# Optimization experiments

Measured on AMD Instinct MI355X. Metric: run time of the kernel, lower is better.

## Reference

```python
import jax, jax.numpy as jnp
import numpy as np

INF = 1e38  # matches torch source constant


def setup_inputs() -> dict:
    key = jax.random.key(0)
    k1, k2, k3 = jax.random.split(key, 3)
    B, N, D = 16, 2048, 512
    query = jax.random.normal(k1, (B, N, D), dtype=jnp.float32)
    # nn.Linear(dims, dims, bias=False): weight [out, in] = [D, D]
    W_in = jax.random.normal(k2, (D, D), dtype=jnp.float32) * (1.0 / np.sqrt(D))
    # nn.Linear(2*dims, dims, bias=False): weight [D, 2D]
    W_out = jax.random.normal(k3, (D, 2 * D), dtype=jnp.float32) * (1.0 / np.sqrt(2 * D))
    return {"query": query, "W_in": W_in, "W_out": W_out}


def reference(query, W_in, W_out):
    B, N, D = query.shape
    # linear_in: y = x @ W^T
    q = jnp.einsum("bnd,ed->bne", query, W_in)  # [B, N, D]
    # full QK^T scores
    scores = jnp.einsum("bnd,bmd->bnm", q, q)  # [B, N, N]
    # torch: scores[:, triu_mask] = -INF  -> mask upper triangle INCLUDING diagonal
    mask = jnp.triu(jnp.ones((N, N), dtype=bool))
    scores = jnp.where(mask, -INF, scores)
    weights = jax.nn.softmax(scores, axis=-1)
    # row 0 is all -INF -> softmax gives uniform; torch zeroes it explicitly
    weights = weights.at[:, 0, :].set(0.0)
    mix = jnp.einsum("bnm,bmd->bnd", weights, q)  # [B, N, D]
    combined = jnp.concatenate([mix, q], axis=-1)  # [B, N, 2D]
    # linear_out (no activation since activation=None)
    output = jnp.einsum("bnc,dc->bnd", combined, W_out)  # [B, N, D]
    return output
```

## Files before the change

kernel.cpp:

```cpp
#include <hip/hip_runtime.h>

typedef _Float16 f16;
typedef _Float16 half8 __attribute__((ext_vector_type(8)));
typedef _Float16 half4 __attribute__((ext_vector_type(4)));
typedef float floatx4 __attribute__((ext_vector_type(4)));

#define MFMA16(a, b, c) __builtin_amdgcn_mfma_f32_16x16x32_f16(a, b, c, 0, 0, 0)

#define PHASE_WAIT_4()  do { asm volatile("s_waitcnt vmcnt(4)" ::: "memory"); \
    __builtin_amdgcn_sched_barrier(0); __builtin_amdgcn_s_barrier(); } while (0)
#define PHASE_WAIT_0()  do { asm volatile("s_waitcnt vmcnt(0)" ::: "memory"); \
    __builtin_amdgcn_sched_barrier(0); __builtin_amdgcn_s_barrier(); } while (0)

__device__ __forceinline__ void gload16(const void* g, void* l) {
    __builtin_amdgcn_global_load_lds((const __attribute__((address_space(1))) void*)g,
                                     (__attribute__((address_space(3))) void*)l, 16, 0, 0);
}


__global__ __launch_bounds__(256) void k_cvt(const float* __restrict__ query,
                                             const float* __restrict__ Wi,
                                             const float* __restrict__ Wo,
                                             f16* __restrict__ q16,
                                             f16* __restrict__ W16)
{
    int i = blockIdx.x * 256 + threadIdx.x;
    const float4* src;
    f16* dst;
    if (i < 4194304) { src = (const float4*)query + i; dst = q16 + (size_t)i * 4; }
    else if (i < 4259840) { int j = i - 4194304; src = (const float4*)Wi + j; dst = W16 + (size_t)j * 4; }
    else { int j = i - 4259840; src = (const float4*)Wo + j; dst = W16 + 262144 + (size_t)j * 4; }
    float4 v = *src;
    half4 h = {(f16)v.x, (f16)v.y, (f16)v.z, (f16)v.w};
    *reinterpret_cast<half4*>(dst) = h;
}

__global__ __launch_bounds__(512, 4) void k_qin(const f16* __restrict__ q16,
                                                const f16* __restrict__ W16,
                                                f16* __restrict__ comb,
                                                f16* __restrict__ qT)
{
    __shared__ char sm[65536];
    const int tid = threadIdx.x, lane = tid & 63, w = tid >> 6;
    const int l15 = lane & 15, quad = lane >> 4;
    const int id = blockIdx.x, xcd = id & 7, u = id >> 3;
    const int mbase = (xcd * 32 + (u >> 2)) * 128;
    const int nbase = (u & 3) * 128;
    const int wm = (w & 1) * 64, wn = (w >> 1) * 32;
    const int ia = (w & 1) * 4, jb = (w >> 1) * 2;

    floatx4 acc[4][2];
#pragma unroll
    for (int i = 0; i < 4; ++i)
#pragma unroll
        for (int j = 0; j < 2; ++j) acc[i][j] = (floatx4)0.f;

    auto STAGE = [&](int k0, int bsel) {
        f16* At = (f16*)(sm + bsel * 32768);
        f16* Bt = At + 8192;
#pragma unroll
        for (int jr = 0; jr < 2; ++jr) {
            int bi = jr * 8 + w, i2 = bi >> 1, s = bi & 1;
            gload16(q16 + (size_t)(mbase + i2 * 16 + l15) * 512 + k0 + s * 32 + quad * 8, At + bi * 512);
            gload16(W16 + (size_t)(nbase + i2 * 16 + l15) * 512 + k0 + s * 32 + quad * 8, Bt + bi * 512);
        }
    };

    STAGE(0, 0);
    STAGE(64, 1);
    for (int it = 0; it < 8; ++it) {
        const int cur = it & 1;
        if (it < 7) PHASE_WAIT_4(); else PHASE_WAIT_0();
        f16* At = (f16*)(sm + cur * 32768);
        f16* Bt = At + 8192;
#pragma unroll
        for (int s = 0; s < 2; ++s) {
            half8 a[4], bf[2];
#pragma unroll
            for (int i = 0; i < 4; ++i)
                a[i] = *reinterpret_cast<half8*>(At + ((ia + i) * 2 + s) * 512 + lane * 8);
#pragma unroll
            for (int j = 0; j < 2; ++j)
                bf[j] = *reinterpret_cast<half8*>(Bt + ((jb + j) * 2 + s) * 512 + lane * 8);
#pragma unroll
            for (int i = 0; i < 4; ++i)
#pragma unroll
                for (int j = 0; j < 2; ++j)
                    acc[i][j] = MFMA16(a[i], bf[j], acc[i][j]);
        }
        __builtin_amdgcn_s_barrier();
        if (it + 2 < 8) STAGE((it + 2) * 64, cur);
    }
    const int bb = mbase >> 11, tb = mbase & 2047;
    f16* ct = (f16*)sm;
#pragma unroll
    for (int i = 0; i < 4; ++i)
#pragma unroll
        for (int j = 0; j < 2; ++j)
#pragma unroll
            for (int r = 0; r < 4; ++r)
                ct[(wm + i * 16 + quad * 4 + r) * 136 + wn + j * 16 + l15] = (f16)acc[i][j][r];
    __syncthreads();
#pragma unroll
    for (int it = 0; it < 4; ++it) {
        int c = it * 512 + tid, r = c >> 4, c8 = (c & 15) << 3;
        *reinterpret_cast<half8*>(comb + (size_t)(mbase + r) * 1024 + 512 + nbase + c8) =
            *reinterpret_cast<half8*>(ct + r * 136 + c8);
    }
    __syncthreads();
#pragma unroll
    for (int i = 0; i < 4; ++i)
#pragma unroll
        for (int j = 0; j < 2; ++j) {
            half4 h = {(f16)acc[i][j][0], (f16)acc[i][j][1], (f16)acc[i][j][2], (f16)acc[i][j][3]};
            *reinterpret_cast<half4*>(ct + (wn + j * 16 + l15) * 136 + wm + i * 16 + quad * 4) = h;
        }
    __syncthreads();
#pragma unroll
    for (int it = 0; it < 4; ++it) {
        int c = it * 512 + tid, dd = c >> 4, tc = (c & 15) << 3;
        *reinterpret_cast<half8*>(qT + ((size_t)bb * 512 + nbase + dd) * 2048 + tb + tc) =
            *reinterpret_cast<half8*>(ct + dd * 136 + tc);
    }
}

__global__ __launch_bounds__(512, 4) void k_sgemmsm(const f16* __restrict__ comb,
                                                    f16* __restrict__ Pd,
                                                    float* __restrict__ Mt,
                                                    float* __restrict__ Lt)
{
    __shared__ char sm[65536];
    const int tid = threadIdx.x, lane = tid & 63, w = tid >> 6;
    const int l15 = lane & 15, quad = lane >> 4;
    const int wm = (w & 1) * 64, wn = (w >> 1) * 32;
    const int ia = (w & 1) * 4, jb = (w >> 1) * 2;

    int bx = blockIdx.y, mt = 0;
    while ((mt + 1) * (mt + 2) / 2 <= bx) ++mt;
    const int nt = bx - mt * (mt + 1) / 2;
    const int b = blockIdx.x;
    const f16* qa = comb + ((size_t)b * 2048 + mt * 128) * 1024 + 512;
    const f16* qb = comb + ((size_t)b * 2048 + nt * 128) * 1024 + 512;

    floatx4 acc[4][2];
#pragma unroll
    for (int i = 0; i < 4; ++i)
#pragma unroll
        for (int j = 0; j < 2; ++j) acc[i][j] = (floatx4)0.f;

    auto STAGE = [&](int k0, int bsel) {
        f16* At = (f16*)(sm + bsel * 32768);
        f16* Bt = At + 8192;
#pragma unroll
        for (int jr = 0; jr < 2; ++jr) {
            int bi = jr * 8 + w, i2 = bi >> 1, s = bi & 1;
            gload16(qa + (size_t)(i2 * 16 + l15) * 1024 + k0 + s * 32 + quad * 8, At + bi * 512);
            gload16(qb + (size_t)(i2 * 16 + l15) * 1024 + k0 + s * 32 + quad * 8, Bt + bi * 512);
        }
    };

    STAGE(0, 0);
    STAGE(64, 1);
    for (int it = 0; it < 8; ++it) {
        const int cur = it & 1;
        if (it < 7) PHASE_WAIT_4(); else PHASE_WAIT_0();
        f16* At = (f16*)(sm + cur * 32768);
        f16* Bt = At + 8192;
#pragma unroll
        for (int s = 0; s < 2; ++s) {
            half8 a[4], bf[2];
#pragma unroll
            for (int i = 0; i < 4; ++i)
                a[i] = *reinterpret_cast<half8*>(At + ((ia + i) * 2 + s) * 512 + lane * 8);
#pragma unroll
            for (int j = 0; j < 2; ++j)
                bf[j] = *reinterpret_cast<half8*>(Bt + ((jb + j) * 2 + s) * 512 + lane * 8);
#pragma unroll
            for (int i = 0; i < 4; ++i)
#pragma unroll
                for (int j = 0; j < 2; ++j)
                    acc[i][j] = MFMA16(a[i], bf[j], acc[i][j]);
        }
        __builtin_amdgcn_s_barrier();
        if (it + 2 < 8) STAGE((it + 2) * 64, cur);
    }

    const bool diag = (nt == mt);
    f16* ct = (f16*)sm;
    float* redm = (float*)(sm + 34816);
    float* reds = (float*)(sm + 36864);
    const int hb = w & 1;

    float wmax[4][4];
#pragma unroll
    for (int i = 0; i < 4; ++i)
#pragma unroll
        for (int r = 0; r < 4; ++r) {
            const int rowl = wm + i * 16 + quad * 4 + r;
            float mm = -1e38f;
#pragma unroll
            for (int j = 0; j < 2; ++j) {
                float v = acc[i][j][r];
                if (diag && (wn + j * 16 + l15) >= rowl) v = -1e38f;
                mm = fmaxf(mm, v);
            }
            mm = fmaxf(mm, __shfl_xor(mm, 1));
            mm = fmaxf(mm, __shfl_xor(mm, 2));
            mm = fmaxf(mm, __shfl_xor(mm, 4));
            mm = fmaxf(mm, __shfl_xor(mm, 8));
            wmax[i][r] = mm;
        }
    if (l15 == 0)
#pragma unroll
        for (int i = 0; i < 4; ++i)
#pragma unroll
            for (int r = 0; r < 4; ++r)
                redm[w * 64 + i * 16 + quad * 4 + r] = wmax[i][r];
    __syncthreads();

#pragma unroll
    for (int i = 0; i < 4; ++i)
#pragma unroll
        for (int r = 0; r < 4; ++r) {
            const int idx = i * 16 + quad * 4 + r;
            const int rowl = wm + idx;
            const float m = fmaxf(fmaxf(redm[hb * 64 + idx], redm[(hb + 2) * 64 + idx]),
                                  fmaxf(redm[(hb + 4) * 64 + idx], redm[(hb + 6) * 64 + idx]));
            float ssum = 0.f;
#pragma unroll
            for (int j = 0; j < 2; ++j) {
                const int col = wn + j * 16 + l15;
                const bool valid = !diag || (col < rowl);
                float e = valid ? __expf(acc[i][j][r] - m) : 0.f;
                ssum += e;
                ct[rowl * 136 + col] = (f16)e;
            }
            ssum += __shfl_xor(ssum, 1);
            ssum += __shfl_xor(ssum, 2);
            ssum += __shfl_xor(ssum, 4);
            ssum += __shfl_xor(ssum, 8);
            wmax[i][r] = ssum;
        }
    if (l15 == 0)
#pragma unroll
        for (int i = 0; i < 4; ++i)
#pragma unroll
            for (int r = 0; r < 4; ++r)
                reds[w * 64 + i * 16 + quad * 4 + r] = wmax[i][r];
    __syncthreads();

    if (tid < 128) {
        const int h2 = tid >> 6, i2 = tid & 63;
        const float mm = fmaxf(fmaxf(redm[h2 * 64 + i2], redm[(h2 + 2) * 64 + i2]),
                               fmaxf(redm[(h2 + 4) * 64 + i2], redm[(h2 + 6) * 64 + i2]));
        const float ll = (reds[h2 * 64 + i2] + reds[(h2 + 2) * 64 + i2])
                       + (reds[(h2 + 4) * 64 + i2] + reds[(h2 + 6) * 64 + i2]);
        const size_t o = (((size_t)b * 16 + nt) << 11) + mt * 128 + tid;
        Mt[o] = mm;
        Lt[o] = ll;
    }
    f16* Pt = Pd + ((size_t)(b * 136 + bx) << 14);
#pragma unroll
    for (int itp = 0; itp < 4; ++itp) {
        int c = itp * 512 + tid, r_ = c >> 4, c8 = (c & 15) << 3;
        *reinterpret_cast<half8*>(Pt + r_ * 128 + c8) =
            *reinterpret_cast<half8*>(ct + r_ * 136 + c8);
    }
}

__global__ __launch_bounds__(256) void k_stats(float* Mt, const float* __restrict__ Lt)
{
    const int b = blockIdx.x, row = blockIdx.y * 256 + threadIdx.x;
    const int mtr = row >> 7;
    float mv[16], lv[16];
    for (int t = 0; t <= mtr; ++t) {
        const size_t o = (((size_t)b * 16 + t) << 11) + row;
        mv[t] = Mt[o];
        lv[t] = Lt[o];
    }
    float M = -1e38f;
    for (int t = 0; t <= mtr; ++t) M = fmaxf(M, mv[t]);
    float l = 0.f;
    for (int t = 0; t <= mtr; ++t) l += lv[t] * __expf(mv[t] - M);
    const float invl = (l > 0.f) ? 1.f / l : 0.f;
    for (int t = 0; t <= mtr; ++t)
        Mt[(((size_t)b * 16 + t) << 11) + row] = __expf(mv[t] - M) * invl;
}

__global__ __launch_bounds__(256) void k_pscale(f16* __restrict__ Pd,
                                               const float* __restrict__ Ft)
{
    int bx = blockIdx.y, mt = 0;
    while ((mt + 1) * (mt + 2) / 2 <= bx) ++mt;
    const int nt = bx - mt * (mt + 1) / 2;
    const int b = blockIdx.x;
    const int tid = threadIdx.x;
    const int row = tid >> 1, c0 = (tid & 1) * 64;
    const float Fv = Ft[(((size_t)b * 16 + nt) << 11) + mt * 128 + row];
    f16* Pt = Pd + ((size_t)(b * 136 + bx) << 14) + (size_t)row * 128 + c0;
#pragma unroll
    for (int c = 0; c < 8; ++c) {
        half8 h = *reinterpret_cast<half8*>(Pt + c * 8);
#pragma unroll
        for (int e = 0; e < 8; ++e) h[e] = (f16)((float)h[e] * Fv);
        *reinterpret_cast<half8*>(Pt + c * 8) = h;
    }
}

__global__ __launch_bounds__(512, 4) void k_pv(const f16* __restrict__ Pd,
                                               const f16* __restrict__ qT,
                                               f16* __restrict__ comb)
{
    __shared__ char sm[65536];
    const int tid = threadIdx.x, lane = tid & 63, w = tid >> 6;
    const int l15 = lane & 15, quad = lane >> 4;
    const int wm = (w & 1) * 64, wn = (w >> 1) * 32;
    const int ia = (w & 1) * 4, jb = (w >> 1) * 2;
    const int id = blockIdx.x;
    const int p = id & 7, nb = (id >> 3) & 3, b = id >> 5;
    const f16* Pdb = Pd + ((size_t)b * 136 << 14);
    const f16* qTb = qT + ((size_t)b * 512 + nb * 128) * 2048;

    for (int t = 0; t < 2; ++t) {
        const int mt = t ? (15 - p) : p;
        const int tb0 = mt * (mt + 1) / 2;
        const int kit = (mt + 1) * 2;

        floatx4 acc[4][2];
#pragma unroll
        for (int i = 0; i < 4; ++i)
#pragma unroll
            for (int j = 0; j < 2; ++j) acc[i][j] = (floatx4)0.f;

        auto STAGE = [&](int it, int bsel) {
            f16* At = (f16*)(sm + bsel * 32768);
            f16* Bt = At + 8192;
            const int k0 = it * 64;
#pragma unroll
            for (int jr = 0; jr < 2; ++jr) {
                int bi = jr * 8 + w, i2 = bi >> 1, s = bi & 1;
                gload16(Pdb + ((size_t)(tb0 + (k0 >> 7)) << 14) + (size_t)(i2 * 16 + l15) * 128
                            + (k0 & 64) + s * 32 + quad * 8,
                        At + bi * 512);
                gload16(qTb + (size_t)(i2 * 16 + l15) * 2048 + k0 + s * 32 + quad * 8, Bt + bi * 512);
            }
        };

        STAGE(0, 0);
        STAGE(1, 1);
        for (int it = 0; it < kit; ++it) {
            const int cur = it & 1;
            if (it < kit - 1) PHASE_WAIT_4(); else PHASE_WAIT_0();
            f16* At = (f16*)(sm + cur * 32768);
            f16* Bt = At + 8192;
#pragma unroll
            for (int s = 0; s < 2; ++s) {
                half8 a[4], bf[2];
#pragma unroll
                for (int i = 0; i < 4; ++i)
                    a[i] = *reinterpret_cast<half8*>(At + ((ia + i) * 2 + s) * 512 + lane * 8);
#pragma unroll
                for (int j = 0; j < 2; ++j)
                    bf[j] = *reinterpret_cast<half8*>(Bt + ((jb + j) * 2 + s) * 512 + lane * 8);
#pragma unroll
                for (int i = 0; i < 4; ++i)
#pragma unroll
                    for (int j = 0; j < 2; ++j)
                        acc[i][j] = MFMA16(a[i], bf[j], acc[i][j]);
            }
            __builtin_amdgcn_s_barrier();
            if (it + 2 < kit) STAGE(it + 2, cur);
        }

        f16* ct = (f16*)sm;
#pragma unroll
        for (int i = 0; i < 4; ++i)
#pragma unroll
            for (int j = 0; j < 2; ++j)
#pragma unroll
                for (int r = 0; r < 4; ++r)
                    ct[(wm + i * 16 + quad * 4 + r) * 136 + wn + j * 16 + l15] = (f16)acc[i][j][r];
        __syncthreads();
#pragma unroll
        for (int it = 0; it < 4; ++it) {
            int c = it * 512 + tid, r = c >> 4, c8 = (c & 15) << 3;
            *reinterpret_cast<half8*>(comb + ((size_t)b * 2048 + mt * 128 + r) * 1024 + nb * 128 + c8) =
                *reinterpret_cast<half8*>(ct + r * 136 + c8);
        }
        __syncthreads();
    }
}

__global__ __launch_bounds__(512, 4) void k_out(const f16* __restrict__ comb,
                                                const f16* __restrict__ Wo16,
                                                float* __restrict__ out)
{
    __shared__ char sm[65536];
    const int tid = threadIdx.x, lane = tid & 63, w = tid >> 6;
    const int l15 = lane & 15, quad = lane >> 4;
    const int id = blockIdx.x, xcd = id & 7, u = id >> 3;
    const int mbase = (xcd * 32 + (u >> 2)) * 128;
    const int nbase = (u & 3) * 128;
    const int wn = (w >> 1) * 32;
    const int ia = (w & 1) * 4, jb = (w >> 1) * 2;

    floatx4 acc[4][2];
#pragma unroll
    for (int i = 0; i < 4; ++i)
#pragma unroll
        for (int j = 0; j < 2; ++j) acc[i][j] = (floatx4)0.f;

    auto STAGE = [&](int k0, int bsel) {
        f16* At = (f16*)(sm + bsel * 32768);
        f16* Bt = At + 8192;
#pragma unroll
        for (int jr = 0; jr < 2; ++jr) {
            int bi = jr * 8 + w, i2 = bi >> 1, s = bi & 1;
            gload16(comb + (size_t)(mbase + i2 * 16 + l15) * 1024 + k0 + s * 32 + quad * 8,
                    At + bi * 512);
            gload16(Wo16 + (size_t)(nbase + i2 * 16 + l15) * 1024 + k0 + s * 32 + quad * 8,
                    Bt + bi * 512);
        }
    };

    STAGE(0, 0);
    STAGE(64, 1);
    for (int it = 0; it < 16; ++it) {
        const int cur = it & 1;
        if (it < 15) PHASE_WAIT_4(); else PHASE_WAIT_0();
        f16* At = (f16*)(sm + cur * 32768);
        f16* Bt = At + 8192;
#pragma unroll
        for (int s = 0; s < 2; ++s) {
            half8 a[4], bf[2];
#pragma unroll
            for (int i = 0; i < 4; ++i)
                a[i] = *reinterpret_cast<half8*>(At + ((ia + i) * 2 + s) * 512 + lane * 8);
#pragma unroll
            for (int j = 0; j < 2; ++j)
                bf[j] = *reinterpret_cast<half8*>(Bt + ((jb + j) * 2 + s) * 512 + lane * 8);
#pragma unroll
            for (int i = 0; i < 4; ++i)
#pragma unroll
                for (int j = 0; j < 2; ++j)
                    acc[i][j] = MFMA16(a[i], bf[j], acc[i][j]);
        }
        __builtin_amdgcn_s_barrier();
        if (it + 2 < 16) STAGE((it + 2) * 64, cur);
    }
    float* cf = (float*)sm;
    for (int pass = 0; pass < 2; ++pass) {
        __syncthreads();
        if ((w & 1) == pass) {
#pragma unroll
            for (int i = 0; i < 4; ++i)
#pragma unroll
                for (int j = 0; j < 2; ++j)
#pragma unroll
                    for (int r = 0; r < 4; ++r)
                        cf[(i * 16 + quad * 4 + r) * 132 + wn + j * 16 + l15] = acc[i][j][r];
        }
        __syncthreads();
#pragma unroll
        for (int it = 0; it < 4; ++it) {
            int c = it * 512 + tid, row = c >> 5, c4 = (c & 31) << 2;
            __builtin_nontemporal_store(
                *reinterpret_cast<floatx4*>(cf + row * 132 + c4),
                reinterpret_cast<floatx4*>(out + (size_t)(mbase + pass * 64 + row) * 512 + nbase + c4));
        }
    }
}

extern "C" void kernel_launch(void* const* d_in, const int* in_sizes, int n_in,
                              void* d_out, int out_size, void* d_ws, size_t ws_size,
                              hipStream_t stream)
{
    const float* query = (const float*)d_in[0];
    const float* W_in  = (const float*)d_in[1];
    const float* W_out = (const float*)d_in[2];
    float* out = (float*)d_out;

    const size_t XOFF = 102236160ull;
    f16* comb = (f16*)d_ws;
    f16* qT   = comb + (size_t)32768 * 1024;
    f16* W16  = qT + (size_t)16 * 512 * 2048;
    f16* q16  = (f16*)((char*)d_ws + XOFF);
    f16* Pd   = (f16*)((char*)d_ws + XOFF);
    float* Mt = (float*)((char*)d_ws + XOFF + 71303168ull);
    float* Lt = (float*)((char*)d_ws + XOFF + 73400320ull);

    k_cvt<<<17152, 256, 0, stream>>>(query, W_in, W_out, q16, W16);
    k_qin<<<1024, 512, 0, stream>>>(q16, W16, comb, qT);
    k_sgemmsm<<<dim3(16, 136), 512, 0, stream>>>(comb, Pd, Mt, Lt);
    k_stats<<<dim3(16, 8), 256, 0, stream>>>(Mt, Lt);
    k_pscale<<<dim3(16, 136), 256, 0, stream>>>(Pd, Mt);
    k_pv<<<512, 512, 0, stream>>>(Pd, qT, comb);
    k_out<<<1024, 512, 0, stream>>>(comb, W16 + 262144, out);
}
```

Measured before the change: 408.4 us.

## Fuse softmax row rescaling into PV GEMM and remap blocks for XCD locality

Removes the separate k_pscale pass that read and rewrote the whole P matrix. The per-tile softmax correction factors now go into LDS, and each 128-column K tile's partial accumulator is scaled and folded into a second accumulator inside k_pv. The score and PV kernels also remap block indices so each batch's blocks land on the same XCD, which should improve L2 reuse. In exchange, k_pv uses more accumulator registers and dynamic shared memory (72 KB), which may cut occupancy, and adds extra vector multiplies every other iteration.

```diff
diff --git a/kernel.cpp b/kernel.cpp
--- a/kernel.cpp
+++ b/kernel.cpp
@@ -135,10 +135,11 @@
     const int wm = (w & 1) * 64, wn = (w >> 1) * 32;
     const int ia = (w & 1) * 4, jb = (w >> 1) * 2;
 
-    int bx = blockIdx.y, mt = 0;
+    const int bhalf = (blockIdx.y >= 136) ? 1 : 0;
+    int bx = blockIdx.y - bhalf * 136, mt = 0;
     while ((mt + 1) * (mt + 2) / 2 <= bx) ++mt;
     const int nt = bx - mt * (mt + 1) / 2;
-    const int b = blockIdx.x;
+    const int b = blockIdx.x + bhalf * 8;
     const f16* qa = comb + ((size_t)b * 2048 + mt * 128) * 1024 + 512;
     const f16* qb = comb + ((size_t)b * 2048 + nt * 128) * 1024 + 512;
 
@@ -287,50 +288,41 @@
         Mt[(((size_t)b * 16 + t) << 11) + row] = __expf(mv[t] - M) * invl;
 }
 
-__global__ __launch_bounds__(256) void k_pscale(f16* __restrict__ Pd,
-                                               const float* __restrict__ Ft)
-{
-    int bx = blockIdx.y, mt = 0;
-    while ((mt + 1) * (mt + 2) / 2 <= bx) ++mt;
-    const int nt = bx - mt * (mt + 1) / 2;
-    const int b = blockIdx.x;
-    const int tid = threadIdx.x;
-    const int row = tid >> 1, c0 = (tid & 1) * 64;
-    const float Fv = Ft[(((size_t)b * 16 + nt) << 11) + mt * 128 + row];
-    f16* Pt = Pd + ((size_t)(b * 136 + bx) << 14) + (size_t)row * 128 + c0;
-#pragma unroll
-    for (int c = 0; c < 8; ++c) {
-        half8 h = *reinterpret_cast<half8*>(Pt + c * 8);
-#pragma unroll
-        for (int e = 0; e < 8; ++e) h[e] = (f16)((float)h[e] * Fv);
-        *reinterpret_cast<half8*>(Pt + c * 8) = h;
-    }
-}
-
 __global__ __launch_bounds__(512, 4) void k_pv(const f16* __restrict__ Pd,
                                                const f16* __restrict__ qT,
-                                               f16* __restrict__ comb)
-{
-    __shared__ char sm[65536];
+                                               f16* __restrict__ comb,
+                                               const float* __restrict__ Ft)
+{
+    extern __shared__ char sm[];
     const int tid = threadIdx.x, lane = tid & 63, w = tid >> 6;
     const int l15 = lane & 15, quad = lane >> 4;
     const int wm = (w & 1) * 64, wn = (w >> 1) * 32;
     const int ia = (w & 1) * 4, jb = (w >> 1) * 2;
     const int id = blockIdx.x;
-    const int p = id & 7, nb = (id >> 3) & 3, b = id >> 5;
+    const int xcd = id & 7, v = id >> 3;
+    const int nb = v & 3, p = (v >> 2) & 7, half_ = v >> 5;
+    const int b = xcd + 8 * half_;
     const f16* Pdb = Pd + ((size_t)b * 136 << 14);
     const f16* qTb = qT + ((size_t)b * 512 + nb * 128) * 2048;
+    float* F_lds = (float*)(sm + 65536);
 
     for (int t = 0; t < 2; ++t) {
         const int mt = t ? (15 - p) : p;
         const int tb0 = mt * (mt + 1) / 2;
         const int kit = (mt + 1) * 2;
 
-        floatx4 acc[4][2];
+        if (tid * 4 < (mt + 1) * 128) {
+            const int idx = tid * 4, tt = idx >> 7, r4 = idx & 127;
+            *reinterpret_cast<floatx4*>(F_lds + idx) =
+                *reinterpret_cast<const floatx4*>(Ft + (((size_t)b * 16 + tt) << 11) + mt * 128 + r4);
+        }
+        __syncthreads();
+
+        floatx4 acc[4][2], accT[4][2];
 #pragma unroll
         for (int i = 0; i < 4; ++i)
 #pragma unroll
-            for (int j = 0; j < 2; ++j) acc[i][j] = (floatx4)0.f;
+            for (int j = 0; j < 2; ++j) { acc[i][j] = (floatx4)0.f; accT[i][j] = (floatx4)0.f; }
 
         auto STAGE = [&](int it, int bsel) {
             f16* At = (f16*)(sm + bsel * 32768);
@@ -368,6 +360,19 @@
                     for (int j = 0; j < 2; ++j)
                         acc[i][j] = MFMA16(a[i], bf[j], acc[i][j]);
             }
+            if (it & 1) {
+                const int tt = it >> 1;
+                const float* fp = F_lds + tt * 128 + wm;
+#pragma unroll
+                for (int i = 0; i < 4; ++i) {
+                    floatx4 fv = *reinterpret_cast<const floatx4*>(fp + i * 16 + quad * 4);
+#pragma unroll
+                    for (int j = 0; j < 2; ++j) {
+                        accT[i][j] += acc[i][j] * fv;
+                        acc[i][j] = (floatx4)0.f;
+                    }
+                }
+            }
             __builtin_amdgcn_s_barrier();
             if (it + 2 < kit) STAGE(it + 2, cur);
         }
@@ -379,7 +384,7 @@
             for (int j = 0; j < 2; ++j)
 #pragma unroll
                 for (int r = 0; r < 4; ++r)
-                    ct[(wm + i * 16 + quad * 4 + r) * 136 + wn + j * 16 + l15] = (f16)acc[i][j][r];
+                    ct[(wm + i * 16 + quad * 4 + r) * 136 + wn + j * 16 + l15] = (f16)accT[i][j][r];
         __syncthreads();
 #pragma unroll
         for (int it = 0; it < 4; ++it) {
@@ -491,9 +496,8 @@
 
     k_cvt<<<17152, 256, 0, stream>>>(query, W_in, W_out, q16, W16);
     k_qin<<<1024, 512, 0, stream>>>(q16, W16, comb, qT);
-    k_sgemmsm<<<dim3(16, 136), 512, 0, stream>>>(comb, Pd, Mt, Lt);
+    k_sgemmsm<<<dim3(8, 272), 512, 0, stream>>>(comb, Pd, Mt, Lt);
     k_stats<<<dim3(16, 8), 256, 0, stream>>>(Mt, Lt);
-    k_pscale<<<dim3(16, 136), 256, 0, stream>>>(Pd, Mt);
-    k_pv<<<512, 512, 0, stream>>>(Pd, qT, comb);
+    k_pv<<<512, 512, 73728, stream>>>(Pd, qT, comb, Mt);
     k_out<<<1024, 512, 0, stream>>>(comb, W16 + 262144, out);
 }
```

After: 373.6 us. -8.5%, faster.
